# Kernel optimization log

Hardware: AMD Instinct MI355X
Metric: run time of the kernel (lower is better)

Reference implementation:

```python
import jax, jax.numpy as jnp
from jax import lax
import numpy as np

B, C, H, W = 16, 1, 1024, 1024


def _erode(x, ksize=3):
    # torch: zero-pad then min over ksize x ksize window
    pad = (ksize - 1) // 2
    xp = jnp.pad(x, ((0, 0), (0, 0), (pad, pad), (pad, pad)))  # constant 0, matches F.pad
    return lax.reduce_window(xp, jnp.array(jnp.inf, x.dtype), lax.min,
                             (1, 1, ksize, ksize), (1, 1, 1, 1), 'VALID')


def _circle_weights(y_true):
    e1 = _erode(y_true)
    e2 = _erode(e1)
    e3 = _erode(e2)
    e4 = _erode(e3)
    circle_all = (0.4 * (y_true - e1) + 0.5 * (e1 - e2)
                  + 0.6 * (e2 - e3) + 0.7 * (e3 - e4))
    circle_all = jnp.where(circle_all == 0, jnp.asarray(0.8, circle_all.dtype), circle_all)
    return lax.stop_gradient(circle_all)  # computed under torch.no_grad()


def setup_inputs() -> dict:
    key = jax.random.key(0)
    k1, k2 = jax.random.split(key)
    y_pred = jax.random.uniform(k1, (B, C, H, W), dtype=jnp.float32)
    # binary-ish segmentation mask so erosion rings are non-trivial
    y_true = (jax.random.uniform(k2, (B, C, H, W)) > 0.7).astype(jnp.float32)
    return {"y_pred": y_pred, "y_true": y_true}


def reference(y_pred, y_true):
    w = _circle_weights(y_true)
    loss = (y_pred - y_true) ** 2 * w  # MSELoss(reduction='none') * weights
    return (loss.mean(axis=(1, 2, 3)), loss.mean())
```

## Files before the change

### kernel.cpp

```cpp
#include <hip/hip_runtime.h>
#include <stdint.h>

#define BATCH 16
#define HH 1024
#define WW 1024
#define TH 8
#define HALO 4
#define ROWS (TH + 2*HALO)
#define WORDS (WW/64)
#define WPAD (WORDS + 1)
#define NTHREADS 256
#define NWAVES (NTHREADS/64)
#define NBLOCKS_MSE (BATCH * (HH / TH))

__global__ __launch_bounds__(NTHREADS) void fused_mse_kernel(
    const float* __restrict__ y_pred,
    const float* __restrict__ y_true,
    float* __restrict__ ws_partial)
{
    __shared__ unsigned long long bits0[ROWS][WPAD];
    __shared__ unsigned long long bufA[ROWS][WPAD];
    __shared__ unsigned long long bufB[ROWS][WPAD];
    __shared__ unsigned long long E[4][TH][WPAD];
    __shared__ float wavesum[NWAVES];

    const int tid  = threadIdx.x;
    const int lane = tid & 63;
    const int wave = tid >> 6;

    const int im = blockIdx.x / (HH / TH);
    const int rb = blockIdx.x % (HH / TH);
    const int r0 = rb * TH - HALO;

    const float* yp = y_pred + (size_t)im * HH * WW;
    const float* yt = y_true + (size_t)im * HH * WW;

    {
        int row  = tid >> 4;
        int word = tid & (WORDS - 1);
        int gr   = r0 + row;
        unsigned long long m = 0ull;
        if (gr >= 0 && gr < HH) {
            const uint4* src = reinterpret_cast<const uint4*>(yt + (size_t)gr * WW + word * 64);
            #pragma unroll
            for (int i = 0; i < 16; ++i) {
                uint4 q = src[i];
                unsigned long long nib = (unsigned long long)(
                    (q.x ? 1u : 0u) | (q.y ? 2u : 0u) | (q.z ? 4u : 0u) | (q.w ? 8u : 0u));
                m |= nib << (4 * i);
            }
        }
        bits0[row][word] = m;
        bufA[row][word]  = m;
    }

    float4 pv[TH];
    #pragma unroll
    for (int row = 0; row < TH; ++row) {
        int gr = r0 + HALO + row;
        pv[row] = *reinterpret_cast<const float4*>(&yp[(size_t)gr * WW + tid * 4]);
    }
    __syncthreads();

    #pragma unroll
    for (int k = 1; k <= 4; ++k) {
        unsigned long long (*src)[WPAD] = (k & 1) ? bufA : bufB;
        unsigned long long (*dst)[WPAD] = (k & 1) ? bufB : bufA;
        int lo = k, hi = ROWS - k;
        int n  = (hi - lo) * WORDS;
        if (tid < n) {
            int row  = lo + (tid >> 4);
            int word = tid & (WORDS - 1);
            unsigned long long h0, h1, h2;
            {
                unsigned long long m = src[row - 1][word];
                unsigned long long l = (word > 0)         ? src[row - 1][word - 1] : 0ull;
                unsigned long long r = (word < WORDS - 1) ? src[row - 1][word + 1] : 0ull;
                h0 = m & ((m << 1) | (l >> 63)) & ((m >> 1) | (r << 63));
            }
            {
                unsigned long long m = src[row][word];
                unsigned long long l = (word > 0)         ? src[row][word - 1] : 0ull;
                unsigned long long r = (word < WORDS - 1) ? src[row][word + 1] : 0ull;
                h1 = m & ((m << 1) | (l >> 63)) & ((m >> 1) | (r << 63));
            }
            {
                unsigned long long m = src[row + 1][word];
                unsigned long long l = (word > 0)         ? src[row + 1][word - 1] : 0ull;
                unsigned long long r = (word < WORDS - 1) ? src[row + 1][word + 1] : 0ull;
                h2 = m & ((m << 1) | (l >> 63)) & ((m >> 1) | (r << 63));
            }
            unsigned long long res = h0 & h1 & h2;
            dst[row][word] = res;
            if (row >= HALO && row < HALO + TH) E[k - 1][row - HALO][word] = res;
        }
        __syncthreads();
    }

    const int word = tid >> 4;
    const int bsh  = (tid & 15) * 4;
    float lsum = 0.0f;
    #pragma unroll
    for (int row = 0; row < TH; ++row) {
        unsigned int y4 = (unsigned int)((bits0[row + HALO][word] >> bsh) & 0xFull);
        unsigned int n1 = (unsigned int)((E[0][row][word] >> bsh) & 0xFull);
        unsigned int n2 = (unsigned int)((E[1][row][word] >> bsh) & 0xFull);
        unsigned int n3 = (unsigned int)((E[2][row][word] >> bsh) & 0xFull);
        unsigned int n4 = (unsigned int)((E[3][row][word] >> bsh) & 0xFull);
        float pvals[4] = {pv[row].x, pv[row].y, pv[row].z, pv[row].w};
        #pragma unroll
        for (int j = 0; j < 4; ++j) {
            unsigned int y = (y4 >> j) & 1u;
            unsigned int c = y + ((n1 >> j) & 1u) + ((n2 >> j) & 1u)
                               + ((n3 >> j) & 1u) + ((n4 >> j) & 1u);
            float w = (c == 0u || c == 5u) ? 0.8f : (0.3f + 0.1f * (float)c);
            float d = pvals[j] - (float)y;
            lsum += d * d * w;
        }
    }

    for (int off = 32; off > 0; off >>= 1)
        lsum += __shfl_down(lsum, off, 64);
    if (lane == 0) wavesum[wave] = lsum;
    __syncthreads();
    if (tid == 0) {
        float s = 0.0f;
        for (int wv = 0; wv < NWAVES; ++wv) s += wavesum[wv];
        ws_partial[blockIdx.x] = s;
    }
}

__global__ __launch_bounds__(NTHREADS) void reduce_kernel(
    const float* __restrict__ partial,
    float* __restrict__ out)
{
    __shared__ float ssum[NTHREADS];
    __shared__ float imsum[BATCH];
    const int tid = threadIdx.x;
    float s = 0.0f;
    #pragma unroll
    for (int j = 0; j < NBLOCKS_MSE / NTHREADS; ++j)
        s += partial[tid * (NBLOCKS_MSE / NTHREADS) + j];
    ssum[tid] = s;
    __syncthreads();
    if (tid < BATCH) {
        float a = 0.0f;
        #pragma unroll
        for (int t = 0; t < NTHREADS / BATCH; ++t)
            a += ssum[tid * (NTHREADS / BATCH) + t];
        imsum[tid] = a;
        out[tid] = a * (1.0f / (float)(HH * WW));
    }
    __syncthreads();
    if (tid == 0) {
        float tot = 0.0f;
        #pragma unroll
        for (int i = 0; i < BATCH; ++i) tot += imsum[i];
        out[BATCH] = tot * (1.0f / ((float)BATCH * (float)(HH * WW)));
    }
}

__global__ __launch_bounds__(NTHREADS) void circle_mse_kernel(
    const float* __restrict__ y_pred,
    const float* __restrict__ y_true,
    float* __restrict__ out)
{
    __shared__ unsigned long long bits0[ROWS][WPAD];
    __shared__ unsigned long long cur[ROWS][WPAD];
    __shared__ unsigned long long tmp[ROWS][WPAD];
    __shared__ unsigned long long E[4][TH][WPAD];
    __shared__ float wavesum[NWAVES];

    const int tid  = threadIdx.x;
    const int lane = tid & 63;
    const int wave = tid >> 6;
    const int im = blockIdx.x / (HH / TH);
    const int rb = blockIdx.x % (HH / TH);
    const int r0 = rb * TH - HALO;
    const float* yt = y_true + (size_t)im * HH * WW;
    const float* yp = y_pred + (size_t)im * HH * WW;

    #pragma unroll 8
    for (int p = wave; p < ROWS * WORDS; p += NWAVES) {
        int row  = p >> 4;
        int word = p & (WORDS - 1);
        int gr   = r0 + row;
        unsigned long long m = 0ull;
        if (gr >= 0 && gr < HH) {
            float v = yt[(size_t)gr * WW + word * 64 + lane];
            m = __ballot(v != 0.0f);
        }
        if (lane == 0) { bits0[row][word] = m; cur[row][word] = m; }
    }
    __syncthreads();

    for (int k = 1; k <= 4; ++k) {
        int lo = k - 1, hi = ROWS - (k - 1);
        for (int p = tid; p < (hi - lo) * WORDS; p += NTHREADS) {
            int row  = lo + (p >> 4);
            int word = p & (WORDS - 1);
            unsigned long long m = cur[row][word];
            unsigned long long l = (word > 0)         ? cur[row][word - 1] : 0ull;
            unsigned long long r = (word < WORDS - 1) ? cur[row][word + 1] : 0ull;
            tmp[row][word] = m & ((m << 1) | (l >> 63)) & ((m >> 1) | (r << 63));
        }
        __syncthreads();
        lo = k; hi = ROWS - k;
        for (int p = tid; p < (hi - lo) * WORDS; p += NTHREADS) {
            int row  = lo + (p >> 4);
            int word = p & (WORDS - 1);
            unsigned long long res = tmp[row - 1][word] & tmp[row][word] & tmp[row + 1][word];
            cur[row][word] = res;
            if (row >= HALO && row < HALO + TH) E[k - 1][row - HALO][word] = res;
        }
        __syncthreads();
    }

    const int word = tid >> 4;
    const int bsh  = (tid & 15) * 4;
    float lsum = 0.0f;
    #pragma unroll
    for (int row = 0; row < TH; ++row) {
        int gr = r0 + HALO + row;
        float4 pv = *reinterpret_cast<const float4*>(&yp[(size_t)gr * WW + tid * 4]);
        unsigned int y4 = (unsigned int)((bits0[row + HALO][word] >> bsh) & 0xFull);
        unsigned int n1 = (unsigned int)((E[0][row][word] >> bsh) & 0xFull);
        unsigned int n2 = (unsigned int)((E[1][row][word] >> bsh) & 0xFull);
        unsigned int n3 = (unsigned int)((E[2][row][word] >> bsh) & 0xFull);
        unsigned int n4 = (unsigned int)((E[3][row][word] >> bsh) & 0xFull);
        float pvals[4] = {pv.x, pv.y, pv.z, pv.w};
        #pragma unroll
        for (int j = 0; j < 4; ++j) {
            unsigned int y = (y4 >> j) & 1u;
            unsigned int c = y + ((n1 >> j) & 1u) + ((n2 >> j) & 1u)
                               + ((n3 >> j) & 1u) + ((n4 >> j) & 1u);
            float w = (c == 0u || c == 5u) ? 0.8f : (0.3f + 0.1f * (float)c);
            float d = pvals[j] - (float)y;
            lsum += d * d * w;
        }
    }
    for (int off = 32; off > 0; off >>= 1)
        lsum += __shfl_down(lsum, off, 64);
    if (lane == 0) wavesum[wave] = lsum;
    __syncthreads();
    if (tid == 0) {
        float s = 0.0f;
        for (int wv = 0; wv < NWAVES; ++wv) s += wavesum[wv];
        atomicAdd(&out[im], s * (1.0f / (float)(HH * WW)));
        atomicAdd(&out[BATCH], s * (1.0f / ((float)BATCH * (float)(HH * WW))));
    }
}

extern "C" void kernel_launch(void* const* d_in, const int* in_sizes, int n_in,
                              void* d_out, int out_size, void* d_ws, size_t ws_size,
                              hipStream_t stream) {
    const float* y_pred = (const float*)d_in[0];
    const float* y_true = (const float*)d_in[1];
    float* out = (float*)d_out;

    const size_t need = (size_t)NBLOCKS_MSE * sizeof(float);
    if (ws_size >= need && d_ws != nullptr) {
        float* ws_partial = (float*)d_ws;
        fused_mse_kernel<<<dim3(NBLOCKS_MSE), NTHREADS, 0, stream>>>(y_pred, y_true, ws_partial);
        reduce_kernel<<<dim3(1), NTHREADS, 0, stream>>>(ws_partial, out);
    } else {
        hipMemsetAsync(d_out, 0, (size_t)out_size * sizeof(float), stream);
        circle_mse_kernel<<<dim3(NBLOCKS_MSE), NTHREADS, 0, stream>>>(y_pred, y_true, out);
    }
}
```

Measured before the change: 151.6 us.

## Split fused kernel into pack/erode count kernel and streaming MSE kernel

The fused kernel is split in two. The first packs y_true into bits, runs the four erosions, and writes a 4-bit per-pixel ring count to a workspace buffer. The second streams y_pred with those counts and reduces the weighted squared error, so y_pred is no longer held in registers across the erosion barriers. This adds an extra launch and workspace traffic (about 8 MB written and read back), and y_true is now rebuilt from the count instead of being read directly.

```diff
diff --git a/kernel.cpp b/kernel.cpp
--- a/kernel.cpp
+++ b/kernel.cpp
@@ -12,27 +12,31 @@
 #define NTHREADS 256
 #define NWAVES (NTHREADS/64)
 #define NBLOCKS_MSE (BATCH * (HH / TH))
-
-__global__ __launch_bounds__(NTHREADS) void fused_mse_kernel(
-    const float* __restrict__ y_pred,
+#define COUNT_WORDS (BATCH * HH * (WW/16))
+
+__device__ __forceinline__ unsigned long long spread16(unsigned int s) {
+    unsigned long long x = s & 0xFFFFull;
+    x = (x | (x << 24)) & 0x000000FF000000FFull;
+    x = (x | (x << 12)) & 0x000F000F000F000Full;
+    x = (x | (x << 6))  & 0x0303030303030303ull;
+    x = (x | (x << 3))  & 0x1111111111111111ull;
+    return x;
+}
+
+__global__ __launch_bounds__(NTHREADS) void pack_erode_kernel(
     const float* __restrict__ y_true,
-    float* __restrict__ ws_partial)
+    unsigned long long* __restrict__ counts)
 {
     __shared__ unsigned long long bits0[ROWS][WPAD];
     __shared__ unsigned long long bufA[ROWS][WPAD];
     __shared__ unsigned long long bufB[ROWS][WPAD];
     __shared__ unsigned long long E[4][TH][WPAD];
-    __shared__ float wavesum[NWAVES];
-
-    const int tid  = threadIdx.x;
-    const int lane = tid & 63;
-    const int wave = tid >> 6;
-
+
+    const int tid = threadIdx.x;
     const int im = blockIdx.x / (HH / TH);
     const int rb = blockIdx.x % (HH / TH);
     const int r0 = rb * TH - HALO;
 
-    const float* yp = y_pred + (size_t)im * HH * WW;
     const float* yt = y_true + (size_t)im * HH * WW;
 
     {
@@ -52,13 +56,6 @@
         }
         bits0[row][word] = m;
         bufA[row][word]  = m;
-    }
-
-    float4 pv[TH];
-    #pragma unroll
-    for (int row = 0; row < TH; ++row) {
-        int gr = r0 + HALO + row;
-        pv[row] = *reinterpret_cast<const float4*>(&yp[(size_t)gr * WW + tid * 4]);
     }
     __syncthreads();
 
@@ -97,24 +94,54 @@
         __syncthreads();
     }
 
-    const int word = tid >> 4;
-    const int bsh  = (tid & 15) * 4;
+    {
+        int row = tid >> 5;
+        int g0  = (tid & 31) * 2;
+        unsigned long long o0 = 0, o1 = 0;
+        #pragma unroll
+        for (int dg = 0; dg < 2; ++dg) {
+            int g    = g0 + dg;
+            int word = g >> 2;
+            int sh   = (g & 3) * 16;
+            unsigned int s0 = (unsigned int)((bits0[row + HALO][word] >> sh) & 0xFFFFull);
+            unsigned int s1 = (unsigned int)((E[0][row][word]      >> sh) & 0xFFFFull);
+            unsigned int s2 = (unsigned int)((E[1][row][word]      >> sh) & 0xFFFFull);
+            unsigned int s3 = (unsigned int)((E[2][row][word]      >> sh) & 0xFFFFull);
+            unsigned int s4 = (unsigned int)((E[3][row][word]      >> sh) & 0xFFFFull);
+            unsigned long long c = spread16(s0) + spread16(s1) + spread16(s2)
+                                 + spread16(s3) + spread16(s4);
+            if (dg == 0) o0 = c; else o1 = c;
+        }
+        size_t base = ((size_t)im * HH + (size_t)(r0 + HALO + row)) * (WW / 16) + g0;
+        ulonglong2 v; v.x = o0; v.y = o1;
+        *reinterpret_cast<ulonglong2*>(&counts[base]) = v;
+    }
+}
+
+__global__ __launch_bounds__(NTHREADS) void mse_kernel(
+    const float* __restrict__ y_pred,
+    const unsigned short* __restrict__ counts16,
+    float* __restrict__ ws_partial)
+{
+    __shared__ float wavesum[NWAVES];
+    const int tid  = threadIdx.x;
+    const int lane = tid & 63;
+    const int wave = tid >> 6;
+    const size_t base = (size_t)blockIdx.x * 2048;
+
     float lsum = 0.0f;
     #pragma unroll
-    for (int row = 0; row < TH; ++row) {
-        unsigned int y4 = (unsigned int)((bits0[row + HALO][word] >> bsh) & 0xFull);
-        unsigned int n1 = (unsigned int)((E[0][row][word] >> bsh) & 0xFull);
-        unsigned int n2 = (unsigned int)((E[1][row][word] >> bsh) & 0xFull);
-        unsigned int n3 = (unsigned int)((E[2][row][word] >> bsh) & 0xFull);
-        unsigned int n4 = (unsigned int)((E[3][row][word] >> bsh) & 0xFull);
-        float pvals[4] = {pv[row].x, pv[row].y, pv[row].z, pv[row].w};
+    for (int it = 0; it < 8; ++it) {
+        size_t idx = base + (size_t)it * NTHREADS + tid;
+        float4 p = reinterpret_cast<const float4*>(y_pred)[idx];
+        unsigned int cs = counts16[idx];
+        float pvals[4] = {p.x, p.y, p.z, p.w};
         #pragma unroll
         for (int j = 0; j < 4; ++j) {
-            unsigned int y = (y4 >> j) & 1u;
-            unsigned int c = y + ((n1 >> j) & 1u) + ((n2 >> j) & 1u)
-                               + ((n3 >> j) & 1u) + ((n4 >> j) & 1u);
+            unsigned int c = (cs >> (4 * j)) & 15u;
+            float y = (c != 0u) ? 1.0f : 0.0f;
             float w = (c == 0u || c == 5u) ? 0.8f : (0.3f + 0.1f * (float)c);
-            float d = pvals[j] - (float)y;
+            float d = pvals[j] - y;
             lsum += d * d * w;
         }
     }
@@ -258,10 +285,14 @@
     const float* y_true = (const float*)d_in[1];
     float* out = (float*)d_out;
 
-    const size_t need = (size_t)NBLOCKS_MSE * sizeof(float);
+    const size_t need = (size_t)COUNT_WORDS * sizeof(unsigned long long)
+                      + (size_t)NBLOCKS_MSE * sizeof(float);
     if (ws_size >= need && d_ws != nullptr) {
-        float* ws_partial = (float*)d_ws;
-        fused_mse_kernel<<<dim3(NBLOCKS_MSE), NTHREADS, 0, stream>>>(y_pred, y_true, ws_partial);
+        unsigned long long* counts = (unsigned long long*)d_ws;
+        float* ws_partial = (float*)(counts + COUNT_WORDS);
+        pack_erode_kernel<<<dim3(NBLOCKS_MSE), NTHREADS, 0, stream>>>(y_true, counts);
+        mse_kernel<<<dim3(NBLOCKS_MSE), NTHREADS, 0, stream>>>(
+            y_pred, (const unsigned short*)counts, ws_partial);
         reduce_kernel<<<dim3(1), NTHREADS, 0, stream>>>(ws_partial, out);
     } else {
         hipMemsetAsync(d_out, 0, (size_t)out_size * sizeof(float), stream);
```

Result: slower. 161.5 us (+6.6%).
